# Optimization experiments

Hardware: AMD Instinct MI355X
Metric: run time of the kernel (lower is better)

## Reference

```python
import jax, jax.numpy as jnp
import numpy as np

B, T = 512, 8192
DT = jnp.float32(1e-3)


def setup_inputs() -> dict:
    key = jax.random.key(0)
    k1, k2, k3, k4 = jax.random.split(key, 4)
    # scale noise so the 8192-step linear recurrence stays well-conditioned
    xicovs = jax.random.normal(k1, (B, T, 2, 2), jnp.float32) * 0.05
    dy = jax.random.normal(k2, (B, T, 2), jnp.float32) * 0.05
    coeffs_A = jax.random.uniform(k3, (2, 2), jnp.float32, -0.05, 0.05)  # 'uniform' init kernel
    C = jax.random.normal(k4, (2, 2), jnp.float32)
    return {"xicovs": xicovs, "dy": dy, "coeffs_A": coeffs_A, "C": C}


def reference(xicovs, dy, coeffs_A, C):
    # xicovs: [B,T,2,2], dy: [B,T,2]
    Bv = xicovs.shape[0]
    # initial state [1,0] broadcast over batch
    x0 = jnp.broadcast_to(jnp.array([1.0, 0.0], jnp.float32), (Bv, 2))
    xi_t = jnp.swapaxes(xicovs, 0, 1)  # [T,B,2,2]
    dy_t = jnp.swapaxes(dy, 0, 1)      # [T,B,2]

    def step(x, inp):
        xic, dyt = inp  # [B,2,2], [B,2]
        # cell emits C @ x_prev * dt
        out = jnp.einsum('ij,bj->bi', C, x) * DT
        A_minus_xiC = coeffs_A - jnp.einsum('bij,jk->bik', xic, C)  # [B,2,2]
        dx = jnp.einsum('bij,bj->bi', A_minus_xiC, x) * DT + jnp.einsum('bij,bj->bi', xic, dyt)
        return x + dx, out

    _, outs = jax.lax.scan(step, x0, (xi_t, dy_t))  # outs: [T,B,2]
    return jnp.swapaxes(outs, 0, 1)  # [B,T,2] (return_sequences=True)
```

## Files before the change

kernel.cpp:

```cpp
#include <hip/hip_runtime.h>


#define B_    512
#define T_    8192
#define LPT   8
#define NT    256
#define CSTEP (NT * LPT)
#define NCHK  (T_ / CSTEP)

struct Aff { float m00, m01, m10, m11, v0, v1; };

__device__ __forceinline__ Aff aff_compose(const Aff& L, const Aff& E) {
    Aff r;
    r.m00 = L.m00*E.m00 + L.m01*E.m10;
    r.m01 = L.m00*E.m01 + L.m01*E.m11;
    r.m10 = L.m10*E.m00 + L.m11*E.m10;
    r.m11 = L.m10*E.m01 + L.m11*E.m11;
    r.v0  = L.m00*E.v0  + L.m01*E.v1 + L.v0;
    r.v1  = L.m10*E.v0  + L.m11*E.v1 + L.v1;
    return r;
}

__device__ __forceinline__ Aff aff_identity() {
    Aff r; r.m00 = 1.f; r.m01 = 0.f; r.m10 = 0.f; r.m11 = 1.f; r.v0 = 0.f; r.v1 = 0.f;
    return r;
}

__global__ __launch_bounds__(NT) void grm_tot(
    const float* __restrict__ xic, const float* __restrict__ dy,
    const float* __restrict__ Aptr, const float* __restrict__ Cptr,
    float* __restrict__ totals)
{
    __shared__ float4 lds4[4 * 256];

    const int blk  = blockIdx.x;
    const int b    = blk / 3;
    const int c    = blk - b * 3;
    const int tid  = threadIdx.x;
    const int lane = tid & 63;
    const int wave = tid >> 6;

    float4* slice = lds4 + wave * 256;

    const float DT = 1e-3f;
    const float cd00 = Cptr[0]*DT, cd01 = Cptr[1]*DT;
    const float cd10 = Cptr[2]*DT, cd11 = Cptr[3]*DT;
    const float i00 = 1.0f + Aptr[0]*DT, i01 = Aptr[1]*DT;
    const float i10 = Aptr[2]*DT,        i11 = 1.0f + Aptr[3]*DT;

    const int wbase = b * T_ + c * CSTEP + wave * 512;
    const float4* xw = (const float4*)xic + wbase;
    const float4* dw = (const float4*)dy  + (wbase >> 1);

    float4 t[8], u[4];
    #pragma unroll
    for (int j = 0; j < 8; ++j) t[j] = xw[j*64 + lane];
    #pragma unroll
    for (int j = 0; j < 4; ++j) u[j] = dw[j*64 + lane];

    float4 a[LPT];
    #pragma unroll
    for (int rr = 0; rr < 2; ++rr) {
        #pragma unroll
        for (int jj = 0; jj < 4; ++jj) {
            int j = 4*rr + jj;
            int f = j*64 + lane;
            int rel = (f >> 3) & 31;
            slice[rel*8 + ((lane & 7) ^ (rel & 7))] = t[j];
        }
        if ((lane >> 5) == rr) {
            int rel = lane & 31;
            #pragma unroll
            for (int s = 0; s < LPT; ++s)
                a[s] = slice[rel*8 + (s ^ (rel & 7))];
        }
    }

    #pragma unroll
    for (int j = 0; j < 4; ++j) {
        int f = j*64 + lane;
        int o = f >> 2;
        slice[o*4 + ((f & 3) ^ ((o >> 1) & 3))] = u[j];
    }
    float4 d[4];
    #pragma unroll
    for (int s = 0; s < 4; ++s)
        d[s] = slice[lane*4 + (s ^ ((lane >> 1) & 3))];

#define STEP_MAPA(i, S_)                                                \
    {                                                                   \
        const float4 x4 = a[i];                                         \
        const float dyx = ((i)&1) ? d[(i)>>1].z : d[(i)>>1].x;          \
        const float dyy = ((i)&1) ? d[(i)>>1].w : d[(i)>>1].y;          \
        (S_).m00 = i00 - (x4.x*cd00 + x4.y*cd10);                       \
        (S_).m01 = i01 - (x4.x*cd01 + x4.y*cd11);                       \
        (S_).m10 = i10 - (x4.z*cd00 + x4.w*cd10);                       \
        (S_).m11 = i11 - (x4.z*cd01 + x4.w*cd11);                       \
        (S_).v0  = x4.x*dyx + x4.y*dyy;                                 \
        (S_).v1  = x4.z*dyx + x4.w*dyy;                                 \
    }

    Aff P;
    STEP_MAPA(0, P);
    #pragma unroll
    for (int i = 1; i < LPT; ++i) { Aff s; STEP_MAPA(i, s); P = aff_compose(s, P); }
#undef STEP_MAPA

    Aff S = P;
    #pragma unroll
    for (int sh = 1; sh < 64; sh <<= 1) {
        Aff q;
        q.m00 = __shfl_up(S.m00, sh); q.m01 = __shfl_up(S.m01, sh);
        q.m10 = __shfl_up(S.m10, sh); q.m11 = __shfl_up(S.m11, sh);
        q.v0  = __shfl_up(S.v0,  sh); q.v1  = __shfl_up(S.v1,  sh);
        if (lane >= sh) S = aff_compose(S, q);
    }

    if (lane == 63) {
        float* h = (float*)slice;
        h[0] = S.m00; h[1] = S.m01; h[2] = S.m10; h[3] = S.m11;
        h[4] = S.v0;  h[5] = S.v1;
    }
    __syncthreads();

    if (tid == 0) {
        Aff Tb = aff_identity();
        #pragma unroll
        for (int w = 0; w < 4; ++w) {
            const float* h = (const float*)(lds4 + w * 256);
            Aff t2;
            t2.m00 = h[0]; t2.m01 = h[1]; t2.m10 = h[2]; t2.m11 = h[3];
            t2.v0  = h[4]; t2.v1  = h[5];
            Tb = aff_compose(t2, Tb);
        }
        float* o = totals + (size_t)blk * 6;
        o[0] = Tb.m00; o[1] = Tb.m01; o[2] = Tb.m10; o[3] = Tb.m11;
        o[4] = Tb.v0;  o[5] = Tb.v1;
    }
}

__global__ __launch_bounds__(NT) void grm_xs(
    const float* __restrict__ totals,
    float2* __restrict__ xs)
{
    const int b = blockIdx.x * NT + threadIdx.x;
    float x0 = 1.0f, x1 = 0.0f;
    float2* xb = xs + (size_t)b * NCHK;
    xb[0] = make_float2(x0, x1);
    for (int c = 0; c < NCHK - 1; ++c) {
        const float* h = totals + ((size_t)b * 3 + c) * 6;
        float nx0 = h[0]*x0 + h[1]*x1 + h[4];
        float nx1 = h[2]*x0 + h[3]*x1 + h[5];
        x0 = nx0; x1 = nx1;
        xb[c + 1] = make_float2(x0, x1);
    }
}

__global__ __launch_bounds__(NT) void grm_emit(
    const float* __restrict__ xic, const float* __restrict__ dy,
    const float* __restrict__ Aptr, const float* __restrict__ Cptr,
    const float2* __restrict__ xs,
    float4* __restrict__ out4)
{
    __shared__ float4 lds4[4 * 256];

    const int blk  = blockIdx.x;
    const int b    = blk >> 2;
    const int c    = blk & (NCHK - 1);
    const int tid  = threadIdx.x;
    const int lane = tid & 63;
    const int wave = tid >> 6;

    float4* slice = lds4 + wave * 256;

    const float DT = 1e-3f;
    const float cd00 = Cptr[0]*DT, cd01 = Cptr[1]*DT;
    const float cd10 = Cptr[2]*DT, cd11 = Cptr[3]*DT;
    const float i00 = 1.0f + Aptr[0]*DT, i01 = Aptr[1]*DT;
    const float i10 = Aptr[2]*DT,        i11 = 1.0f + Aptr[3]*DT;

    const float2 xbv = xs[blk];
    const float xb0 = xbv.x, xb1 = xbv.y;

    const int wbase = b * T_ + c * CSTEP + wave * 512;
    const float4* xw = (const float4*)xic + wbase;
    const float4* dw = (const float4*)dy  + (wbase >> 1);
    float4*       ow = out4 + (wbase >> 1);

    float4 t[8], u[4];
    #pragma unroll
    for (int j = 0; j < 8; ++j) t[j] = xw[j*64 + lane];
    #pragma unroll
    for (int j = 0; j < 4; ++j) u[j] = dw[j*64 + lane];

    float4 a[LPT];
    #pragma unroll
    for (int rr = 0; rr < 2; ++rr) {
        #pragma unroll
        for (int jj = 0; jj < 4; ++jj) {
            int j = 4*rr + jj;
            int f = j*64 + lane;
            int rel = (f >> 3) & 31;
            slice[rel*8 + ((lane & 7) ^ (rel & 7))] = t[j];
        }
        if ((lane >> 5) == rr) {
            int rel = lane & 31;
            #pragma unroll
            for (int s = 0; s < LPT; ++s)
                a[s] = slice[rel*8 + (s ^ (rel & 7))];
        }
    }

    #pragma unroll
    for (int j = 0; j < 4; ++j) {
        int f = j*64 + lane;
        int o = f >> 2;
        slice[o*4 + ((f & 3) ^ ((o >> 1) & 3))] = u[j];
    }
    float4 d[4];
    #pragma unroll
    for (int s = 0; s < 4; ++s)
        d[s] = slice[lane*4 + (s ^ ((lane >> 1) & 3))];

#define STEP_MAPB(i, S_)                                                \
    {                                                                   \
        const float4 x4 = a[i];                                         \
        const float dyx = ((i)&1) ? d[(i)>>1].z : d[(i)>>1].x;          \
        const float dyy = ((i)&1) ? d[(i)>>1].w : d[(i)>>1].y;          \
        (S_).m00 = i00 - (x4.x*cd00 + x4.y*cd10);                       \
        (S_).m01 = i01 - (x4.x*cd01 + x4.y*cd11);                       \
        (S_).m10 = i10 - (x4.z*cd00 + x4.w*cd10);                       \
        (S_).m11 = i11 - (x4.z*cd01 + x4.w*cd11);                       \
        (S_).v0  = x4.x*dyx + x4.y*dyy;                                 \
        (S_).v1  = x4.z*dyx + x4.w*dyy;                                 \
    }

    Aff P;
    STEP_MAPB(0, P);
    #pragma unroll
    for (int i = 1; i < LPT; ++i) { Aff s; STEP_MAPB(i, s); P = aff_compose(s, P); }

    Aff S = P;
    #pragma unroll
    for (int sh = 1; sh < 64; sh <<= 1) {
        Aff q;
        q.m00 = __shfl_up(S.m00, sh); q.m01 = __shfl_up(S.m01, sh);
        q.m10 = __shfl_up(S.m10, sh); q.m11 = __shfl_up(S.m11, sh);
        q.v0  = __shfl_up(S.v0,  sh); q.v1  = __shfl_up(S.v1,  sh);
        if (lane >= sh) S = aff_compose(S, q);
    }

    if (lane == 63) {
        float* h = (float*)slice;
        h[0] = S.m00; h[1] = S.m01; h[2] = S.m10; h[3] = S.m11;
        h[4] = S.v0;  h[5] = S.v1;
    }
    __syncthreads();

    Aff Ew = aff_identity();
    for (int w = 0; w < wave; ++w) {
        const float* h = (const float*)(lds4 + w * 256);
        Aff t2;
        t2.m00 = h[0]; t2.m01 = h[1]; t2.m10 = h[2]; t2.m11 = h[3];
        t2.v0  = h[4]; t2.v1  = h[5];
        Ew = aff_compose(t2, Ew);
    }

    Aff El;
    El.m00 = __shfl_up(S.m00, 1); El.m01 = __shfl_up(S.m01, 1);
    El.m10 = __shfl_up(S.m10, 1); El.m11 = __shfl_up(S.m11, 1);
    El.v0  = __shfl_up(S.v0,  1); El.v1  = __shfl_up(S.v1,  1);
    if (lane == 0) El = aff_identity();
    Aff E = aff_compose(El, Ew);

    __syncthreads();

    float x0 = E.m00*xb0 + E.m01*xb1 + E.v0;
    float x1 = E.m10*xb0 + E.m11*xb1 + E.v1;

    float4 o4[4];
    #pragma unroll
    for (int i = 0; i < LPT; ++i) {
        float oxx = cd00*x0 + cd01*x1;
        float oyy = cd10*x0 + cd11*x1;
        if (i & 1) { o4[i>>1].z = oxx; o4[i>>1].w = oyy; }
        else       { o4[i>>1].x = oxx; o4[i>>1].y = oyy; }
        Aff s; STEP_MAPB(i, s);
        float nx0 = s.m00*x0 + s.m01*x1 + s.v0;
        float nx1 = s.m10*x0 + s.m11*x1 + s.v1;
        x0 = nx0; x1 = nx1;
    }
#undef STEP_MAPB

    #pragma unroll
    for (int s = 0; s < 4; ++s)
        slice[lane*4 + (s ^ ((lane >> 1) & 3))] = o4[s];
    #pragma unroll
    for (int j = 0; j < 4; ++j) {
        int f = j*64 + lane;
        int o = f >> 2;
        ow[f] = slice[o*4 + ((f & 3) ^ ((o >> 1) & 3))];
    }
}

extern "C" void kernel_launch(void* const* d_in, const int* in_sizes, int n_in,
                              void* d_out, int out_size, void* d_ws, size_t ws_size,
                              hipStream_t stream) {
    const float* xic  = (const float*)d_in[0];
    const float* dy   = (const float*)d_in[1];
    const float* Aptr = (const float*)d_in[2];
    const float* Cptr = (const float*)d_in[3];
    float4* out = (float4*)d_out;

    char* ws = (char*)d_ws;
    float*  totals = (float*)ws;
    float2* xs     = (float2*)(ws + 40960);

    grm_tot <<<B_ * 3,    NT, 0, stream>>>(xic, dy, Aptr, Cptr, totals);
    grm_xs  <<<B_ / NT,   NT, 0, stream>>>(totals, xs);
    grm_emit<<<B_ * NCHK, NT, 0, stream>>>(xic, dy, Aptr, Cptr, xs, out);
}
```

Before: 150.1 us.

## Fuse three-kernel scan into one cooperative kernel with grid sync

Replaces the totals/prefix/emit three-kernel pipeline with a single cooperative kernel. Each block computes its chunk's affine prefix and keeps it in registers, writes the chunk total, waits at a grid-wide sync, then composes the preceding chunk totals itself and emits outputs. This is meant to remove two kernel launches and the second read of xicovs. The cost is a grid barrier, a serial walk over prior chunk totals per block, and a requirement that all 2048 blocks are co-resident (8 per CU), with the old path kept as a fallback.

```diff
diff --git a/kernel.cpp b/kernel.cpp
--- a/kernel.cpp
+++ b/kernel.cpp
@@ -1,4 +1,7 @@
 #include <hip/hip_runtime.h>
+#include <hip/hip_cooperative_groups.h>
+
+namespace cg = cooperative_groups;
 
 
 #define B_    512
@@ -7,6 +10,7 @@
 #define NT    256
 #define CSTEP (NT * LPT)
 #define NCHK  (T_ / CSTEP)
+#define NBLK  (B_ * NCHK)
 
 struct Aff { float m00, m01, m10, m11, v0, v1; };
 
@@ -26,68 +30,7 @@
     return r;
 }
 
-__global__ __launch_bounds__(NT) void grm_tot(
-    const float* __restrict__ xic, const float* __restrict__ dy,
-    const float* __restrict__ Aptr, const float* __restrict__ Cptr,
-    float* __restrict__ totals)
-{
-    __shared__ float4 lds4[4 * 256];
-
-    const int blk  = blockIdx.x;
-    const int b    = blk / 3;
-    const int c    = blk - b * 3;
-    const int tid  = threadIdx.x;
-    const int lane = tid & 63;
-    const int wave = tid >> 6;
-
-    float4* slice = lds4 + wave * 256;
-
-    const float DT = 1e-3f;
-    const float cd00 = Cptr[0]*DT, cd01 = Cptr[1]*DT;
-    const float cd10 = Cptr[2]*DT, cd11 = Cptr[3]*DT;
-    const float i00 = 1.0f + Aptr[0]*DT, i01 = Aptr[1]*DT;
-    const float i10 = Aptr[2]*DT,        i11 = 1.0f + Aptr[3]*DT;
-
-    const int wbase = b * T_ + c * CSTEP + wave * 512;
-    const float4* xw = (const float4*)xic + wbase;
-    const float4* dw = (const float4*)dy  + (wbase >> 1);
-
-    float4 t[8], u[4];
-    #pragma unroll
-    for (int j = 0; j < 8; ++j) t[j] = xw[j*64 + lane];
-    #pragma unroll
-    for (int j = 0; j < 4; ++j) u[j] = dw[j*64 + lane];
-
-    float4 a[LPT];
-    #pragma unroll
-    for (int rr = 0; rr < 2; ++rr) {
-        #pragma unroll
-        for (int jj = 0; jj < 4; ++jj) {
-            int j = 4*rr + jj;
-            int f = j*64 + lane;
-            int rel = (f >> 3) & 31;
-            slice[rel*8 + ((lane & 7) ^ (rel & 7))] = t[j];
-        }
-        if ((lane >> 5) == rr) {
-            int rel = lane & 31;
-            #pragma unroll
-            for (int s = 0; s < LPT; ++s)
-                a[s] = slice[rel*8 + (s ^ (rel & 7))];
-        }
-    }
-
-    #pragma unroll
-    for (int j = 0; j < 4; ++j) {
-        int f = j*64 + lane;
-        int o = f >> 2;
-        slice[o*4 + ((f & 3) ^ ((o >> 1) & 3))] = u[j];
-    }
-    float4 d[4];
-    #pragma unroll
-    for (int s = 0; s < 4; ++s)
-        d[s] = slice[lane*4 + (s ^ ((lane >> 1) & 3))];
-
-#define STEP_MAPA(i, S_)                                                \
+#define STEP_MAP(i, S_)                                                 \
     {                                                                   \
         const float4 x4 = a[i];                                         \
         const float dyx = ((i)&1) ? d[(i)>>1].z : d[(i)>>1].x;          \
@@ -100,11 +43,247 @@
         (S_).v1  = x4.z*dyx + x4.w*dyy;                                 \
     }
 
+__global__ __launch_bounds__(NT, 8) void grm_coop(
+    const float* __restrict__ xic, const float* __restrict__ dy,
+    const float* __restrict__ Aptr, const float* __restrict__ Cptr,
+    float* __restrict__ totals,
+    float4* __restrict__ out4)
+{
+    __shared__ float4 lds4[4 * 256];
+
+    const int blk  = blockIdx.x;
+    const int b    = blk >> 2;
+    const int c    = blk & (NCHK - 1);
+    const int tid  = threadIdx.x;
+    const int lane = tid & 63;
+    const int wave = tid >> 6;
+
+    float4* slice = lds4 + wave * 256;
+
+    const float DT = 1e-3f;
+    const float cd00 = Cptr[0]*DT, cd01 = Cptr[1]*DT;
+    const float cd10 = Cptr[2]*DT, cd11 = Cptr[3]*DT;
+    const float i00 = 1.0f + Aptr[0]*DT, i01 = Aptr[1]*DT;
+    const float i10 = Aptr[2]*DT,        i11 = 1.0f + Aptr[3]*DT;
+
+    const int wbase = b * T_ + c * CSTEP + wave * 512;
+    const float4* xw = (const float4*)xic + wbase;
+    const float4* dw = (const float4*)dy  + (wbase >> 1);
+    float4*       ow = out4 + (wbase >> 1);
+
+    float4 a[LPT];
+    {
+        float4 t[8];
+        #pragma unroll
+        for (int j = 0; j < 8; ++j) t[j] = xw[j*64 + lane];
+        #pragma unroll
+        for (int rr = 0; rr < 2; ++rr) {
+            #pragma unroll
+            for (int jj = 0; jj < 4; ++jj) {
+                int j = 4*rr + jj;
+                int f = j*64 + lane;
+                int rel = (f >> 3) & 31;
+                slice[rel*8 + ((lane & 7) ^ (rel & 7))] = t[j];
+            }
+            if ((lane >> 5) == rr) {
+                int rel = lane & 31;
+                #pragma unroll
+                for (int s = 0; s < LPT; ++s)
+                    a[s] = slice[rel*8 + (s ^ (rel & 7))];
+            }
+        }
+    }
+
+    Aff S;
+    {
+        float4 u[4];
+        #pragma unroll
+        for (int j = 0; j < 4; ++j) u[j] = dw[j*64 + lane];
+        #pragma unroll
+        for (int j = 0; j < 4; ++j) {
+            int f = j*64 + lane;
+            int o = f >> 2;
+            slice[o*4 + ((f & 3) ^ ((o >> 1) & 3))] = u[j];
+        }
+        float4 d[4];
+        #pragma unroll
+        for (int s = 0; s < 4; ++s)
+            d[s] = slice[lane*4 + (s ^ ((lane >> 1) & 3))];
+
+        Aff P;
+        STEP_MAP(0, P);
+        #pragma unroll
+        for (int i = 1; i < LPT; ++i) { Aff s; STEP_MAP(i, s); P = aff_compose(s, P); }
+
+        S = P;
+        #pragma unroll
+        for (int sh = 1; sh < 64; sh <<= 1) {
+            Aff q;
+            q.m00 = __shfl_up(S.m00, sh); q.m01 = __shfl_up(S.m01, sh);
+            q.m10 = __shfl_up(S.m10, sh); q.m11 = __shfl_up(S.m11, sh);
+            q.v0  = __shfl_up(S.v0,  sh); q.v1  = __shfl_up(S.v1,  sh);
+            if (lane >= sh) S = aff_compose(S, q);
+        }
+    }
+
+    if (lane == 63) {
+        float* h = (float*)slice;
+        h[0] = S.m00; h[1] = S.m01; h[2] = S.m10; h[3] = S.m11;
+        h[4] = S.v0;  h[5] = S.v1;
+    }
+    __syncthreads();
+
+    Aff Ew = aff_identity();
+    for (int w = 0; w < wave; ++w) {
+        const float* h = (const float*)(lds4 + w * 256);
+        Aff t2;
+        t2.m00 = h[0]; t2.m01 = h[1]; t2.m10 = h[2]; t2.m11 = h[3];
+        t2.v0  = h[4]; t2.v1  = h[5];
+        Ew = aff_compose(t2, Ew);
+    }
+
+    if (tid == 0) {
+        Aff Tb = aff_identity();
+        #pragma unroll
+        for (int w = 0; w < 4; ++w) {
+            const float* h = (const float*)(lds4 + w * 256);
+            Aff t2;
+            t2.m00 = h[0]; t2.m01 = h[1]; t2.m10 = h[2]; t2.m11 = h[3];
+            t2.v0  = h[4]; t2.v1  = h[5];
+            Tb = aff_compose(t2, Tb);
+        }
+        float* o = totals + (size_t)blk * 6;
+        o[0] = Tb.m00; o[1] = Tb.m01; o[2] = Tb.m10; o[3] = Tb.m11;
+        o[4] = Tb.v0;  o[5] = Tb.v1;
+    }
+
+    Aff E;
+    {
+        Aff El;
+        El.m00 = __shfl_up(S.m00, 1); El.m01 = __shfl_up(S.m01, 1);
+        El.m10 = __shfl_up(S.m10, 1); El.m11 = __shfl_up(S.m11, 1);
+        El.v0  = __shfl_up(S.v0,  1); El.v1  = __shfl_up(S.v1,  1);
+        if (lane == 0) El = aff_identity();
+        E = aff_compose(El, Ew);
+    }
+
+    cg::this_grid().sync();
+
+    float xb0 = 1.0f, xb1 = 0.0f;
+    for (int w = 0; w < c; ++w) {
+        const float* h = totals + ((size_t)(b * NCHK + w)) * 6;
+        float nx0 = h[0]*xb0 + h[1]*xb1 + h[4];
+        float nx1 = h[2]*xb0 + h[3]*xb1 + h[5];
+        xb0 = nx0; xb1 = nx1;
+    }
+
+    float x0 = E.m00*xb0 + E.m01*xb1 + E.v0;
+    float x1 = E.m10*xb0 + E.m11*xb1 + E.v1;
+
+    float4 d[4];
+    {
+        float4 u[4];
+        #pragma unroll
+        for (int j = 0; j < 4; ++j) u[j] = dw[j*64 + lane];
+        #pragma unroll
+        for (int j = 0; j < 4; ++j) {
+            int f = j*64 + lane;
+            int o = f >> 2;
+            slice[o*4 + ((f & 3) ^ ((o >> 1) & 3))] = u[j];
+        }
+        #pragma unroll
+        for (int s = 0; s < 4; ++s)
+            d[s] = slice[lane*4 + (s ^ ((lane >> 1) & 3))];
+    }
+
+    float4 o4[4];
+    #pragma unroll
+    for (int i = 0; i < LPT; ++i) {
+        float oxx = cd00*x0 + cd01*x1;
+        float oyy = cd10*x0 + cd11*x1;
+        if (i & 1) { o4[i>>1].z = oxx; o4[i>>1].w = oyy; }
+        else       { o4[i>>1].x = oxx; o4[i>>1].y = oyy; }
+        Aff s; STEP_MAP(i, s);
+        float nx0 = s.m00*x0 + s.m01*x1 + s.v0;
+        float nx1 = s.m10*x0 + s.m11*x1 + s.v1;
+        x0 = nx0; x1 = nx1;
+    }
+
+    #pragma unroll
+    for (int s = 0; s < 4; ++s)
+        slice[lane*4 + (s ^ ((lane >> 1) & 3))] = o4[s];
+    #pragma unroll
+    for (int j = 0; j < 4; ++j) {
+        int f = j*64 + lane;
+        int o = f >> 2;
+        ow[f] = slice[o*4 + ((f & 3) ^ ((o >> 1) & 3))];
+    }
+}
+
+__global__ __launch_bounds__(NT) void grm_tot(
+    const float* __restrict__ xic, const float* __restrict__ dy,
+    const float* __restrict__ Aptr, const float* __restrict__ Cptr,
+    float* __restrict__ totals)
+{
+    __shared__ float4 lds4[4 * 256];
+
+    const int blk  = blockIdx.x;
+    const int b    = blk / 3;
+    const int c    = blk - b * 3;
+    const int tid  = threadIdx.x;
+    const int lane = tid & 63;
+    const int wave = tid >> 6;
+    float4* slice = lds4 + wave * 256;
+
+    const float DT = 1e-3f;
+    const float cd00 = Cptr[0]*DT, cd01 = Cptr[1]*DT;
+    const float cd10 = Cptr[2]*DT, cd11 = Cptr[3]*DT;
+    const float i00 = 1.0f + Aptr[0]*DT, i01 = Aptr[1]*DT;
+    const float i10 = Aptr[2]*DT,        i11 = 1.0f + Aptr[3]*DT;
+
+    const int wbase = b * T_ + c * CSTEP + wave * 512;
+    const float4* xw = (const float4*)xic + wbase;
+    const float4* dw = (const float4*)dy  + (wbase >> 1);
+
+    float4 t[8], u[4];
+    #pragma unroll
+    for (int j = 0; j < 8; ++j) t[j] = xw[j*64 + lane];
+    #pragma unroll
+    for (int j = 0; j < 4; ++j) u[j] = dw[j*64 + lane];
+
+    float4 a[LPT];
+    #pragma unroll
+    for (int rr = 0; rr < 2; ++rr) {
+        #pragma unroll
+        for (int jj = 0; jj < 4; ++jj) {
+            int j = 4*rr + jj;
+            int f = j*64 + lane;
+            int rel = (f >> 3) & 31;
+            slice[rel*8 + ((lane & 7) ^ (rel & 7))] = t[j];
+        }
+        if ((lane >> 5) == rr) {
+            int rel = lane & 31;
+            #pragma unroll
+            for (int s = 0; s < LPT; ++s)
+                a[s] = slice[rel*8 + (s ^ (rel & 7))];
+        }
+    }
+
+    #pragma unroll
+    for (int j = 0; j < 4; ++j) {
+        int f = j*64 + lane;
+        int o = f >> 2;
+        slice[o*4 + ((f & 3) ^ ((o >> 1) & 3))] = u[j];
+    }
+    float4 d[4];
+    #pragma unroll
+    for (int s = 0; s < 4; ++s)
+        d[s] = slice[lane*4 + (s ^ ((lane >> 1) & 3))];
+
     Aff P;
-    STEP_MAPA(0, P);
-    #pragma unroll
-    for (int i = 1; i < LPT; ++i) { Aff s; STEP_MAPA(i, s); P = aff_compose(s, P); }
-#undef STEP_MAPA
+    STEP_MAP(0, P);
+    #pragma unroll
+    for (int i = 1; i < LPT; ++i) { Aff s; STEP_MAP(i, s); P = aff_compose(s, P); }
 
     Aff S = P;
     #pragma unroll
@@ -170,7 +349,6 @@
     const int tid  = threadIdx.x;
     const int lane = tid & 63;
     const int wave = tid >> 6;
-
     float4* slice = lds4 + wave * 256;
 
     const float DT = 1e-3f;
@@ -222,23 +400,10 @@
     for (int s = 0; s < 4; ++s)
         d[s] = slice[lane*4 + (s ^ ((lane >> 1) & 3))];
 
-#define STEP_MAPB(i, S_)                                                \
-    {                                                                   \
-        const float4 x4 = a[i];                                         \
-        const float dyx = ((i)&1) ? d[(i)>>1].z : d[(i)>>1].x;          \
-        const float dyy = ((i)&1) ? d[(i)>>1].w : d[(i)>>1].y;          \
-        (S_).m00 = i00 - (x4.x*cd00 + x4.y*cd10);                       \
-        (S_).m01 = i01 - (x4.x*cd01 + x4.y*cd11);                       \
-        (S_).m10 = i10 - (x4.z*cd00 + x4.w*cd10);                       \
-        (S_).m11 = i11 - (x4.z*cd01 + x4.w*cd11);                       \
-        (S_).v0  = x4.x*dyx + x4.y*dyy;                                 \
-        (S_).v1  = x4.z*dyx + x4.w*dyy;                                 \
-    }
-
     Aff P;
-    STEP_MAPB(0, P);
-    #pragma unroll
-    for (int i = 1; i < LPT; ++i) { Aff s; STEP_MAPB(i, s); P = aff_compose(s, P); }
+    STEP_MAP(0, P);
+    #pragma unroll
+    for (int i = 1; i < LPT; ++i) { Aff s; STEP_MAP(i, s); P = aff_compose(s, P); }
 
     Aff S = P;
     #pragma unroll
@@ -285,12 +450,11 @@
         float oyy = cd10*x0 + cd11*x1;
         if (i & 1) { o4[i>>1].z = oxx; o4[i>>1].w = oyy; }
         else       { o4[i>>1].x = oxx; o4[i>>1].y = oyy; }
-        Aff s; STEP_MAPB(i, s);
+        Aff s; STEP_MAP(i, s);
         float nx0 = s.m00*x0 + s.m01*x1 + s.v0;
         float nx1 = s.m10*x0 + s.m11*x1 + s.v1;
         x0 = nx0; x1 = nx1;
     }
-#undef STEP_MAPB
 
     #pragma unroll
     for (int s = 0; s < 4; ++s)
@@ -312,11 +476,22 @@
     const float* Cptr = (const float*)d_in[3];
     float4* out = (float4*)d_out;
 
-    char* ws = (char*)d_ws;
-    float*  totals = (float*)ws;
-    float2* xs     = (float2*)(ws + 40960);
-
-    grm_tot <<<B_ * 3,    NT, 0, stream>>>(xic, dy, Aptr, Cptr, totals);
-    grm_xs  <<<B_ / NT,   NT, 0, stream>>>(totals, xs);
-    grm_emit<<<B_ * NCHK, NT, 0, stream>>>(xic, dy, Aptr, Cptr, xs, out);
-}
+    int nb = 0;
+    hipError_t qe = hipOccupancyMaxActiveBlocksPerMultiprocessor(&nb, grm_coop, NT, 0);
+    const bool coop_ok = (qe == hipSuccess) && (nb >= 8);
+
+    if (coop_ok) {
+        float* totals = (float*)d_ws;
+        void* args[] = { (void*)&xic, (void*)&dy, (void*)&Aptr, (void*)&Cptr,
+                         (void*)&totals, (void*)&out };
+        hipLaunchCooperativeKernel((void*)grm_coop, dim3(NBLK), dim3(NT),
+                                   args, 0, stream);
+    } else {
+        char* ws = (char*)d_ws;
+        float*  totals = (float*)ws;
+        float2* xs     = (float2*)(ws + 40960);
+        grm_tot <<<B_ * 3,    NT, 0, stream>>>(xic, dy, Aptr, Cptr, totals);
+        grm_xs  <<<B_ / NT,   NT, 0, stream>>>(totals, xs);
+        grm_emit<<<B_ * NCHK, NT, 0, stream>>>(xic, dy, Aptr, Cptr, xs, out);
+    }
+}
```

Result: no change. 149.3 us (-0.5%).
